# Kernel tuning notes

Measured on AMD Instinct MI355X. Metric: run time of the kernel, lower is better.

## Reference

```python
import jax, jax.numpy as jnp
import numpy as np

G = 4  # groupsize((1,1)) = 4 -> C4 rotations, exact rot90 path


def _lift_filter(w):
    # w: (O, I, k, k) -> (O*G, I, k, k); orbit of 90-degree filter rotations
    f = jnp.stack([jnp.rot90(w, r, axes=(-2, -1)) for r in range(G)], axis=1)
    O, _, I, k, _ = f.shape
    return f.reshape(O * G, I, k, k)


def _group_filter(w):
    # w: (O, I, G, k, k) -> (O*G, I*G, k, k)
    # rotatestack_n: spatial rot90 by r, then cyclic shift of the group axis by r
    fs = []
    for r in range(G):
        roty = jnp.rot90(w, r, axes=(-2, -1))
        roty = jnp.roll(roty, r, axis=-3)  # new[i] = roty[(G - r + i) % G]
        fs.append(roty)
    f = jnp.stack(fs, axis=1)  # (O, G, I, G, k, k)
    O, _, I, _, k, _ = f.shape
    return f.reshape(O * G, I * G, k, k)


def _conv(x, f, b, pad):
    y = jax.lax.conv_general_dilated(x, f, (1, 1), [(pad, pad), (pad, pad)],
                                     dimension_numbers=('NCHW', 'OIHW', 'NCHW'))
    # bias is stacked per group element: repeat each out-channel bias G times
    return y + jnp.repeat(b, G)[None, :, None, None]


def _pool(x):
    return jax.lax.reduce_window(x, -jnp.inf, jax.lax.max, (1, 1, 2, 2), (1, 1, 2, 2), 'VALID')


def setup_inputs():
    key = jax.random.key(0)
    ks = jax.random.split(key, 16)
    ch = [6, 12, 12, 24, 24, 16]   # [24,48,48,96,96,64] // G
    kern = [7, 5, 5, 5, 5, 5]
    d = {'x': jax.random.normal(ks[0], (64, 1, 96, 96), jnp.float32)}
    d['w0'] = jax.random.normal(ks[1], (ch[0], 1, kern[0], kern[0]), jnp.float32) / np.sqrt(ch[0] * 1.0)
    d['b0'] = jnp.zeros((ch[0],), jnp.float32)
    for i in range(1, 6):
        std = 1.0 / np.sqrt(float(ch[i] * ch[i - 1]))
        d['w%d' % i] = jax.random.normal(ks[1 + i], (ch[i], ch[i - 1], G, kern[i], kern[i]), jnp.float32) * std
        d['b%d' % i] = jnp.zeros((ch[i],), jnp.float32)
    d['fw1'] = jax.random.normal(ks[8], (64, 64), jnp.float32) * 0.05
    d['fb1'] = jnp.zeros((64,), jnp.float32)
    d['fw2'] = jax.random.normal(ks[9], (10, 64), jnp.float32) * 0.05
    d['fb2'] = jnp.zeros((10,), jnp.float32)
    return d


def reference(x, w0, b0, w1, b1, w2, b2, w3, b3, w4, b4, w5, b5, fw1, fb1, fw2, fb2):
    h = jax.nn.relu(_conv(x, _lift_filter(w0), b0, 1))                  # (B,24,92,92)
    h = jax.nn.relu(_conv(h, _group_filter(w1), b1, 2))
    h = _pool(h)                                                        # (B,48,46,46)
    h = jax.nn.relu(_conv(h, _group_filter(w2), b2, 2))
    h = jax.nn.relu(_conv(h, _group_filter(w3), b3, 2))
    h = _pool(h)                                                        # (B,96,23,23)
    h = jax.nn.relu(_conv(h, _group_filter(w4), b4, 2))
    h = jax.nn.relu(_conv(h, _group_filter(w5), b5, 1))                 # (B,64,21,21)
    h = h.mean(axis=(-2, -1))                                           # (B,64) flat (out_ch*G)
    h = jax.nn.relu(h @ fw1.T + fb1)
    return h @ fw2.T + fb2                                              # (B,10)
```

## Files before the change

kernel.cpp:

```cpp
#include <hip/hip_runtime.h>
#include <hip/hip_bf16.h>


typedef short s16x8 __attribute__((ext_vector_type(8)));
typedef __bf16 bf16x8 __attribute__((ext_vector_type(8)));
typedef float f32x4 __attribute__((ext_vector_type(4)));
typedef unsigned short u16;

__device__ __forceinline__ u16 f2bf(float f) {
    unsigned u = __float_as_uint(f);
    return (u16)((u + 0x7FFFu + ((u >> 16) & 1u)) >> 16);
}
__device__ __forceinline__ float bf2f(u16 h) {
    return __uint_as_float(((unsigned)h) << 16);
}

__device__ __forceinline__ void rot_src(int r, int K, int y, int x, int& sy, int& sx) {
    switch (r & 3) {
        case 0: sy = y;         sx = x;         break;
        case 1: sy = x;         sx = K - 1 - y; break;
        case 2: sy = K - 1 - y; sx = K - 1 - x; break;
        default: sy = K - 1 - x; sx = y;        break;
    }
}

__global__ void lift_w0T_kernel(const float* __restrict__ w, float* __restrict__ f) {
    const int K = 7, KK = 49, OC = 24;
    int idx = blockIdx.x * blockDim.x + threadIdx.x;
    if (idx >= KK * OC) return;
    int oc = idx % OC; int kk = idx / OC;
    int y = kk / K, x = kk % K;
    int r = oc & 3, o = oc >> 2;
    int sy, sx; rot_src(r, K, y, x, sy, sx);
    f[idx] = w[o * KK + sy * K + sx];
}

__global__ void wfrag_kernel(const float* __restrict__ w, u16* __restrict__ wf,
                             int O, int I, int KC, int NT, int total) {
    int idx = blockIdx.x * blockDim.x + threadIdx.x;
    if (idx >= total) return;
    int j = idx & 7;
    int lane = (idx >> 3) & 63;
    int rest = idx >> 9;
    int nc = rest % NT; rest /= NT;
    int kc = rest % KC; int kpos = rest / KC;
    int ky = kpos / 5, kx = kpos % 5;
    int kk = ((lane >> 4) << 3) + j;
    int ic = kc * 32 + kk;
    int oc = nc * 16 + (lane & 15);
    float val = 0.f;
    if (ic < I * 4) {
        int o = oc >> 2, r = oc & 3, i = ic >> 2, s = ic & 3;
        int g = (s - r + 4) & 3;
        int sy, sx; rot_src(r, 5, ky, kx, sy, sx);
        val = w[(((o * I + i) * 4 + g) * 25) + sy * 5 + sx];
    }
    u16 hb = f2bf(val);
    u16 lb = f2bf(val - bf2f(hb));
    wf[idx] = hb;
    wf[idx + total] = lb;
}

__global__ void pad_x_kernel(const float* __restrict__ x, float* __restrict__ xp) {
    int idx = blockIdx.x * blockDim.x + threadIdx.x;
    if (idx >= 64 * 96 * 96) return;
    int c = idx % 96; int t = idx / 96;
    int r = t % 96; int n = t / 96;
    xp[((size_t)n * 98 + r + 1) * 100 + c + 1] = x[idx];
}

__global__ void prep_pad_kernel(u16* __restrict__ buf, long LO, int NHW,
                                int Hp, int Wp, int ICO, int CR8) {
    int idx = blockIdx.x * blockDim.x + threadIdx.x;
    if (idx >= NHW) return;
    int c = idx % Wp; int t = idx / Wp;
    int r = t % Hp; int n = t / Hp;
    bool halo = (r < 2) || (r >= Hp - 2) || (c < 2) || (c >= Wp - 2);
    int c0 = halo ? 0 : CR8, c1 = ICO >> 3;
    if (c0 >= c1) return;
    size_t base = (((size_t)n * Hp + r) * Wp + c) * ICO;
    s16x8 z = {0, 0, 0, 0, 0, 0, 0, 0};
    for (int cc = c0; cc < c1; ++cc) {
        *(s16x8*)(buf + base + cc * 8) = z;
        *(s16x8*)(buf + LO + base + cc * 8) = z;
    }
}

__global__ __launch_bounds__(256) void conv0_kernel(
        const float* __restrict__ xp, const float* __restrict__ f0t,
        const float* __restrict__ b0, u16* __restrict__ p1, long p1LO) {
    int idx = blockIdx.x * blockDim.x + threadIdx.x;
    if (idx >= 64 * 92 * 23) return;
    int xq = idx % 23; int t = idx / 23;
    int oy = t % 92; int n = t / 92;
    float acc[24][4];
#pragma unroll
    for (int a = 0; a < 24; ++a)
#pragma unroll
        for (int b = 0; b < 4; ++b) acc[a][b] = 0.f;

    const float* ip = xp + ((size_t)n * 98 + oy) * 100 + xq * 4;
#pragma unroll
    for (int ky = 0; ky < 7; ++ky) {
        const float* row = ip + (size_t)ky * 100;
        float xv[12];
#pragma unroll
        for (int v = 0; v < 3; ++v)
            *reinterpret_cast<float4*>(&xv[4 * v]) =
                *reinterpret_cast<const float4*>(row + 4 * v);
#pragma unroll
        for (int kx = 0; kx < 7; ++kx) {
            const float* wp = f0t + (ky * 7 + kx) * 24;
#pragma unroll
            for (int qd = 0; qd < 6; ++qd) {
                float4 wv = *reinterpret_cast<const float4*>(wp + qd * 4);
#pragma unroll
                for (int jx = 0; jx < 4; ++jx) {
                    acc[qd * 4 + 0][jx] = fmaf(wv.x, xv[kx + jx], acc[qd * 4 + 0][jx]);
                    acc[qd * 4 + 1][jx] = fmaf(wv.y, xv[kx + jx], acc[qd * 4 + 1][jx]);
                    acc[qd * 4 + 2][jx] = fmaf(wv.z, xv[kx + jx], acc[qd * 4 + 2][jx]);
                    acc[qd * 4 + 3][jx] = fmaf(wv.w, xv[kx + jx], acc[qd * 4 + 3][jx]);
                }
            }
        }
    }
    float bv[6];
#pragma unroll
    for (int qd = 0; qd < 6; ++qd) bv[qd] = b0[qd];

    size_t ob = (((size_t)n * 96 + oy + 2) * 96 + xq * 4 + 2) * 32;
#pragma unroll
    for (int jx = 0; jx < 4; ++jx) {
        s16x8 hv[4], lv[4];
#pragma unroll
        for (int cc = 0; cc < 3; ++cc)
#pragma unroll
            for (int e = 0; e < 8; ++e) {
                int ch = cc * 8 + e;
                float v = fmaxf(acc[ch][jx] + bv[ch >> 2], 0.f);
                u16 hb = f2bf(v);
                u16 lb = f2bf(v - bf2f(hb));
                hv[cc][e] = (short)hb; lv[cc][e] = (short)lb;
            }
        hv[3] = s16x8{0,0,0,0,0,0,0,0}; lv[3] = s16x8{0,0,0,0,0,0,0,0};
#pragma unroll
        for (int cc = 0; cc < 4; ++cc) {
            *(s16x8*)(p1 + ob + jx * 32 + cc * 8) = hv[cc];
            *(s16x8*)(p1 + p1LO + ob + jx * 32 + cc * 8) = lv[cc];
        }
    }
}

template <int IC32, int NT, int NTW, int MT, int CR, int SW, bool POOL, int XOFF>
__global__ __launch_bounds__(SW*(NT/NTW)*64, 2) void conv_mfma_kernel(
        const u16* __restrict__ act, long actLO,
        const u16* __restrict__ wf, int wfLO,
        const float* __restrict__ bias,
        u16* __restrict__ outP, long outLO,
        float* __restrict__ outF,
        int Hp, int Wp, int OH, int OW, int PH, int POW,
        int NRG, int NXS, int HpO, int WpO, int IC32O) {
    constexpr int OG = NT / NTW;
    constexpr int NW = SW * OG;
    constexpr int KC = IC32 / 32;
    constexpr int WT = MT * 16 + 4 + XOFF;
    constexpr int R  = CR * SW + 4;
    constexpr int CHUNKS = R * WT * 8;
    __shared__ u16 lds[CHUNKS * 8];

    int q8 = gridDim.x >> 3;
    int wid = (blockIdx.x & 7) * q8 + (blockIdx.x >> 3);
    int xs = wid % NXS; int t = wid / NXS;
    int rgrp = t % NRG; int n = t / NRG;

    int BR = rgrp * (CR * SW);
    int rbase = BR + XOFF;
    int xbase = xs * (MT * 16);

    int tid = threadIdx.x;
    int wv = tid >> 6;
    int lane = tid & 63;
    int l15 = lane & 15, lg = lane >> 4;
    int og = wv % OG, rg = wv / OG;

    f32x4 accP[CR][MT][NTW], accQ[CR][MT][NTW];
#pragma unroll
    for (int cr = 0; cr < CR; ++cr)
#pragma unroll
        for (int m = 0; m < MT; ++m)
#pragma unroll
            for (int nc = 0; nc < NTW; ++nc) {
                accP[cr][m][nc] = f32x4{0.f, 0.f, 0.f, 0.f};
                accQ[cr][m][nc] = f32x4{0.f, 0.f, 0.f, 0.f};
            }

    const u16* wfl = wf + (size_t)lane * 8;
    const u16* actn = act + ((size_t)n * Hp) * Wp * IC32;

    for (int kcp = 0; kcp < KC; ++kcp) {
        if (kcp) __syncthreads();
        for (int u = tid; u < CHUNKS; u += NW * 64) {
            int c = u & 7; int rest = u >> 3;
            int xl = rest % WT; int row = rest / WT;
            int cg = c ^ (xl & 7);
            int sp = cg >> 2, cc4 = cg & 3;
            int gx = xbase + xl, gr = rbase + row;
            s16x8 v = {0, 0, 0, 0, 0, 0, 0, 0};
            if (gx < Wp && gr < Hp)
                v = *(const s16x8*)(actn + (size_t)sp * actLO +
                      ((size_t)gr * Wp + gx) * IC32 + (kcp * 4 + cc4) * 8);
            *(s16x8*)&lds[(size_t)u * 8] = v;
        }
        __syncthreads();

        for (int ky = 0; ky < 5; ++ky) {
            for (int kx = 0; kx < 5; ++kx) {
                int kpos = ky * 5 + kx;
                bf16x8 bh[NTW], bl[NTW];
#pragma unroll
                for (int nc = 0; nc < NTW; ++nc) {
                    const u16* bp = wfl +
                        ((size_t)(kpos * KC + kcp) * NT + og * NTW + nc) * 512;
                    bh[nc] = *(const bf16x8*)bp;
                    bl[nc] = *(const bf16x8*)(bp + wfLO);
                }
#pragma unroll
                for (int m = 0; m < MT; ++m) {
                    int xl = m * 16 + XOFF + l15 + kx;
                    int sw = xl & 7;
                    bf16x8 ah[CR], al[CR];
#pragma unroll
                    for (int cr = 0; cr < CR; ++cr) {
                        int row = rg * CR + cr + ky;
                        int base = (row * WT + xl) * 8;
                        ah[cr] = *(const bf16x8*)&lds[(size_t)(base + (lg ^ sw)) * 8];
                        al[cr] = *(const bf16x8*)&lds[(size_t)(base + ((4 + lg) ^ sw)) * 8];
                    }
#pragma unroll
                    for (int nc = 0; nc < NTW; ++nc)
#pragma unroll
                        for (int cr = 0; cr < CR; ++cr) {
                            accP[cr][m][nc] = __builtin_amdgcn_mfma_f32_16x16x32_bf16(
                                ah[cr], bh[nc], accP[cr][m][nc], 0, 0, 0);
                            accQ[cr][m][nc] = __builtin_amdgcn_mfma_f32_16x16x32_bf16(
                                ah[cr], bl[nc], accQ[cr][m][nc], 0, 0, 0);
                            accQ[cr][m][nc] = __builtin_amdgcn_mfma_f32_16x16x32_bf16(
                                al[cr], bh[nc], accQ[cr][m][nc], 0, 0, 0);
                        }
                }
            }
        }
    }

#pragma unroll
    for (int nc = 0; nc < NTW; ++nc) {
        int oc = (og * NTW + nc) * 16 + l15;
        float bv = bias[oc >> 2];
#pragma unroll
        for (int m = 0; m < MT; ++m) {
            int gx0 = xbase + m * 16;
            if constexpr (POOL) {
                int p = rgrp * SW + rg;
                if (p < PH) {
                    float c0[4], c1[4];
#pragma unroll
                    for (int j = 0; j < 4; ++j) {
                        c0[j] = accP[0][m][nc][j] + accQ[0][m][nc][j];
                        c1[j] = accP[1][m][nc][j] + accQ[1][m][nc][j];
                    }
#pragma unroll
                    for (int a2 = 0; a2 < 2; ++a2) {
                        int px = (gx0 + lg * 4 + 2 * a2) >> 1;
                        if (px < POW) {
                            float mx = fmaxf(fmaxf(c0[2 * a2], c0[2 * a2 + 1]),
                                             fmaxf(c1[2 * a2], c1[2 * a2 + 1]));
                            float v = fmaxf(mx + bv, 0.f);
                            u16 hb = f2bf(v);
                            u16 lb = f2bf(v - bf2f(hb));
                            size_t o = (((size_t)n * HpO + p + 2) * WpO + px + 2) * IC32O + oc;
                            outP[o] = hb; outP[o + outLO] = lb;
                        }
                    }
                }
            } else {
#pragma unroll
                for (int cr = 0; cr < CR; ++cr) {
                    int oy = BR + rg * CR + cr;
                    if (oy < OH) {
#pragma unroll
                        for (int j = 0; j < 4; ++j) {
                            int gx = gx0 + lg * 4 + j;
                            if (gx < OW) {
                                float v = fmaxf(accP[cr][m][nc][j] + accQ[cr][m][nc][j] + bv, 0.f);
                                if (outF) {
                                    outF[(((size_t)n * OH + oy) * OW + gx) * (NT * 16) + oc] = v;
                                } else {
                                    u16 hb = f2bf(v);
                                    u16 lb = f2bf(v - bf2f(hb));
                                    size_t o = (((size_t)n * HpO + oy + 2) * WpO + gx + 2) * IC32O + oc;
                                    outP[o] = hb; outP[o + outLO] = lb;
                                }
                            }
                        }
                    }
                }
            }
        }
    }
}

__global__ void mean_nhwc_kernel(const float* __restrict__ in, float* __restrict__ out) {
    __shared__ float sm[256];
    int n = blockIdx.x;
    int c = threadIdx.x & 63, q = threadIdx.x >> 6;
    float s = 0.f;
    for (int p = q; p < 441; p += 4) s += in[((size_t)n * 441 + p) * 64 + c];
    sm[threadIdx.x] = s;
    __syncthreads();
    if (q == 0) out[n * 64 + c] = (sm[c] + sm[c + 64] + sm[c + 128] + sm[c + 192]) * (1.0f / 441.0f);
}

__global__ void fc_kernel(const float* __restrict__ mean, const float* __restrict__ fw1,
                          const float* __restrict__ fb1, const float* __restrict__ fw2,
                          const float* __restrict__ fb2, float* __restrict__ out) {
    __shared__ float m[4096];
    __shared__ float h1[4096];
    int tid = threadIdx.x;
    for (int i = tid; i < 4096; i += 256) m[i] = mean[i];
    __syncthreads();
    for (int i = tid; i < 4096; i += 256) {
        int n = i >> 6, j = i & 63;
        float s = fb1[j];
        for (int k = 0; k < 64; ++k) s = fmaf(m[n * 64 + k], fw1[j * 64 + k], s);
        h1[i] = fmaxf(s, 0.f);
    }
    __syncthreads();
    for (int i = tid; i < 640; i += 256) {
        int n = i / 10, j2 = i % 10;
        float s = fb2[j2];
        for (int j = 0; j < 64; ++j) s = fmaf(h1[n * 64 + j], fw2[j2 * 64 + j], s);
        out[i] = s;
    }
}

extern "C" void kernel_launch(void* const* d_in, const int* in_sizes, int n_in,
                              void* d_out, int out_size, void* d_ws, size_t ws_size,
                              hipStream_t stream) {
    const float* x   = (const float*)d_in[0];
    const float* w0  = (const float*)d_in[1];
    const float* b0  = (const float*)d_in[2];
    const float* w1  = (const float*)d_in[3];
    const float* b1  = (const float*)d_in[4];
    const float* w2  = (const float*)d_in[5];
    const float* b2  = (const float*)d_in[6];
    const float* w3  = (const float*)d_in[7];
    const float* b3  = (const float*)d_in[8];
    const float* w4  = (const float*)d_in[9];
    const float* b4  = (const float*)d_in[10];
    const float* w5  = (const float*)d_in[11];
    const float* b5  = (const float*)d_in[12];
    const float* fw1 = (const float*)d_in[13];
    const float* fb1 = (const float*)d_in[14];
    const float* fw2 = (const float*)d_in[15];
    const float* fb2 = (const float*)d_in[16];

    char* ws = (char*)d_ws;
    if (ws_size < 128827392ull) return;

    float* F0   = (float*)(ws + 0);
    u16*   WF1  = (u16*)(ws + 8192);
    u16*   WF2  = (u16*)(ws + 161792);
    u16*   WF3  = (u16*)(ws + 468992);
    u16*   WF4  = (u16*)(ws + 1083392);
    u16*   WF5  = (u16*)(ws + 2004992);
    float* MEANB= (float*)(ws + 2619392);
    float* XP   = (float*)(ws + 2635776);
    float* C5   = (float*)(ws + 5144576);
    u16*   A    = (u16*)(ws + 12369920);
    u16*   B    = (u16*)(ws + 87867392);
    const long P1LO = 18874368;
    const long P2LO = 10240000;
    const long P4LO = 4478976;

    hipLaunchKernelGGL(lift_w0T_kernel, dim3(5), dim3(256), 0, stream, w0, F0);
    hipLaunchKernelGGL(wfrag_kernel, dim3(150), dim3(256), 0, stream, w1, WF1, 12, 6, 1, 3, 38400);
    hipLaunchKernelGGL(wfrag_kernel, dim3(300), dim3(256), 0, stream, w2, WF2, 12, 12, 2, 3, 76800);
    hipLaunchKernelGGL(wfrag_kernel, dim3(600), dim3(256), 0, stream, w3, WF3, 24, 12, 2, 6, 153600);
    hipLaunchKernelGGL(wfrag_kernel, dim3(900), dim3(256), 0, stream, w4, WF4, 24, 24, 3, 6, 230400);
    hipLaunchKernelGGL(wfrag_kernel, dim3(600), dim3(256), 0, stream, w5, WF5, 16, 24, 3, 4, 153600);

    hipMemsetAsync(XP, 0, 2508800, stream);
    hipLaunchKernelGGL(pad_x_kernel, dim3(2304), dim3(256), 0, stream, x, XP);

    hipLaunchKernelGGL(prep_pad_kernel, dim3((64*96*96 + 255)/256), dim3(256), 0, stream,
                       A, P1LO, 64*96*96, 96, 96, 32, 4);
    hipLaunchKernelGGL(conv0_kernel, dim3((64*92*23 + 255)/256), dim3(256), 0, stream,
                       XP, F0, b0, A, P1LO);

    hipLaunchKernelGGL(prep_pad_kernel, dim3((64*50*50 + 255)/256), dim3(256), 0, stream,
                       B, P2LO, 64*50*50, 50, 50, 64, 6);
    hipLaunchKernelGGL((conv_mfma_kernel<32, 3, 3, 3, 2, 4, true, 0>), dim3(1536), dim3(256), 0, stream,
                       A, P1LO, WF1, 38400, b1, B, P2LO, (float*)nullptr,
                       96, 96, 92, 92, 46, 46, 12, 2, 50, 50, 64);

    hipLaunchKernelGGL(prep_pad_kernel, dim3((64*50*50 + 255)/256), dim3(256), 0, stream,
                       A, P2LO, 64*50*50, 50, 50, 64, 6);
    hipLaunchKernelGGL((conv_mfma_kernel<64, 3, 3, 3, 1, 4, false, 0>), dim3(768), dim3(256), 0, stream,
                       B, P2LO, WF2, 76800, b2, A, P2LO, (float*)nullptr,
                       50, 50, 46, 46, 0, 0, 12, 1, 50, 50, 64);

    hipLaunchKernelGGL(prep_pad_kernel, dim3((64*27*27 + 255)/256), dim3(256), 0, stream,
                       B, P4LO, 64*27*27, 27, 27, 96, 12);
    hipLaunchKernelGGL((conv_mfma_kernel<64, 6, 3, 3, 2, 2, true, 0>), dim3(768), dim3(256), 0, stream,
                       A, P2LO, WF3, 153600, b3, B, P4LO, (float*)nullptr,
                       50, 50, 46, 46, 23, 23, 12, 1, 27, 27, 96);

    hipLaunchKernelGGL(prep_pad_kernel, dim3((64*27*27 + 255)/256), dim3(256), 0, stream,
                       A, P4LO, 64*27*27, 27, 27, 96, 12);
    hipLaunchKernelGGL((conv_mfma_kernel<96, 6, 3, 2, 2, 2, false, 0>), dim3(384), dim3(256), 0, stream,
                       B, P4LO, WF4, 230400, b4, A, P4LO, (float*)nullptr,
                       27, 27, 23, 23, 0, 0, 6, 1, 27, 27, 96);

    hipLaunchKernelGGL((conv_mfma_kernel<96, 4, 2, 2, 2, 2, false, 1>), dim3(384), dim3(256), 0, stream,
                       A, P4LO, WF5, 153600, b5, (u16*)A, 0, C5,
                       27, 27, 21, 21, 0, 0, 6, 1, 27, 27, 96);

    hipLaunchKernelGGL(mean_nhwc_kernel, dim3(64), dim3(256), 0, stream, C5, MEANB);
    hipLaunchKernelGGL(fc_kernel, dim3(1), dim3(256), 0, stream,
                       MEANB, fw1, fb1, fw2, fb2, (float*)d_out);
}
```

Before: 677.4 us.

## Stage conv epilogue through LDS for coalesced vector stores and shrink padded buffers

Conv epilogues now write their bf16 hi/lo results into shared memory first, then write them out to the padded NHWC buffer with 16-byte coalesced stores, instead of scattered 2-byte stores. The first activation buffer is stored with 24 channels instead of zero-padded 32, and the conv kernel zero-fills the missing channels when loading. The prep kernels now zero only the halo. The main conv loops are fully unrolled and occupancy hints are raised for some layers. The LDS staging adds an extra barrier and shared-memory traffic, and the unrolling may raise register pressure.

New measurement: 1.478 ms. 2.18x slower.

```diff
diff --git a/kernel.cpp b/kernel.cpp
--- a/kernel.cpp
+++ b/kernel.cpp
@@ -6,6 +6,7 @@
 typedef __bf16 bf16x8 __attribute__((ext_vector_type(8)));
 typedef float f32x4 __attribute__((ext_vector_type(4)));
 typedef unsigned short u16;
+typedef unsigned int u32;
 
 __device__ __forceinline__ u16 f2bf(float f) {
     unsigned u = __float_as_uint(f);
@@ -69,18 +70,17 @@
     xp[((size_t)n * 98 + r + 1) * 100 + c + 1] = x[idx];
 }
 
-__global__ void prep_pad_kernel(u16* __restrict__ buf, long LO, int NHW,
-                                int Hp, int Wp, int ICO, int CR8) {
+__global__ void prep_halo_kernel(u16* __restrict__ buf, long LO, int NHW,
+                                 int Hp, int Wp, int ICO) {
     int idx = blockIdx.x * blockDim.x + threadIdx.x;
     if (idx >= NHW) return;
     int c = idx % Wp; int t = idx / Wp;
     int r = t % Hp; int n = t / Hp;
     bool halo = (r < 2) || (r >= Hp - 2) || (c < 2) || (c >= Wp - 2);
-    int c0 = halo ? 0 : CR8, c1 = ICO >> 3;
-    if (c0 >= c1) return;
+    if (!halo) return;
     size_t base = (((size_t)n * Hp + r) * Wp + c) * ICO;
     s16x8 z = {0, 0, 0, 0, 0, 0, 0, 0};
-    for (int cc = c0; cc < c1; ++cc) {
+    for (int cc = 0; cc < (ICO >> 3); ++cc) {
         *(s16x8*)(buf + base + cc * 8) = z;
         *(s16x8*)(buf + LO + base + cc * 8) = z;
     }
@@ -128,10 +128,10 @@
 #pragma unroll
     for (int qd = 0; qd < 6; ++qd) bv[qd] = b0[qd];
 
-    size_t ob = (((size_t)n * 96 + oy + 2) * 96 + xq * 4 + 2) * 32;
+    size_t ob = (((size_t)n * 96 + oy + 2) * 96 + xq * 4 + 2) * 24;
 #pragma unroll
     for (int jx = 0; jx < 4; ++jx) {
-        s16x8 hv[4], lv[4];
+        s16x8 hv[3], lv[3];
 #pragma unroll
         for (int cc = 0; cc < 3; ++cc)
 #pragma unroll
@@ -142,36 +142,43 @@
                 u16 lb = f2bf(v - bf2f(hb));
                 hv[cc][e] = (short)hb; lv[cc][e] = (short)lb;
             }
-        hv[3] = s16x8{0,0,0,0,0,0,0,0}; lv[3] = s16x8{0,0,0,0,0,0,0,0};
-#pragma unroll
-        for (int cc = 0; cc < 4; ++cc) {
-            *(s16x8*)(p1 + ob + jx * 32 + cc * 8) = hv[cc];
-            *(s16x8*)(p1 + p1LO + ob + jx * 32 + cc * 8) = lv[cc];
-        }
-    }
-}
-
-template <int IC32, int NT, int NTW, int MT, int CR, int SW, bool POOL, int XOFF>
-__global__ __launch_bounds__(SW*(NT/NTW)*64, 2) void conv_mfma_kernel(
+#pragma unroll
+        for (int cc = 0; cc < 3; ++cc) {
+            *(s16x8*)(p1 + ob + jx * 24 + cc * 8) = hv[cc];
+            *(s16x8*)(p1 + p1LO + ob + jx * 24 + cc * 8) = lv[cc];
+        }
+    }
+}
+
+template <int IC32, int ICIN, int NT, int NTW, int MT, int CR, int SW, bool POOL,
+          int XOFF, int OCO, bool TRANS, int MINW>
+__global__ __launch_bounds__(SW*(NT/NTW)*64, MINW) void conv_mfma_kernel(
         const u16* __restrict__ act, long actLO,
         const u16* __restrict__ wf, int wfLO,
         const float* __restrict__ bias,
         u16* __restrict__ outP, long outLO,
         float* __restrict__ outF,
         int Hp, int Wp, int OH, int OW, int PH, int POW,
-        int NRG, int NXS, int HpO, int WpO, int IC32O) {
+        int NRG, int NXS, int HpO, int WpO) {
     constexpr int OG = NT / NTW;
     constexpr int NW = SW * OG;
     constexpr int KC = IC32 / 32;
     constexpr int WT = MT * 16 + 4 + XOFF;
     constexpr int R  = CR * SW + 4;
     constexpr int CHUNKS = R * WT * 8;
-    __shared__ u16 lds[CHUNKS * 8];
+    constexpr int TROWS = POOL ? SW : CR * SW;
+    constexpr int TX = POOL ? MT * 8 : MT * 16;
+    constexpr int SX = OCO + 4;
+    constexpr int STAGE_B = CHUNKS * 16;
+    constexpr int TRAN_B = TRANS ? TROWS * TX * SX * 4 : 0;
+    constexpr int LDSB = STAGE_B > TRAN_B ? STAGE_B : TRAN_B;
+    __shared__ __align__(16) char ldsraw[LDSB];
+    u16* lds = (u16*)ldsraw;
 
     int q8 = gridDim.x >> 3;
     int wid = (blockIdx.x & 7) * q8 + (blockIdx.x >> 3);
-    int xs = wid % NXS; int t = wid / NXS;
-    int rgrp = t % NRG; int n = t / NRG;
+    int xs = wid % NXS; int t0 = wid / NXS;
+    int rgrp = t0 % NRG; int n = t0 / NRG;
 
     int BR = rgrp * (CR * SW);
     int rbase = BR + XOFF;
@@ -195,7 +202,7 @@
             }
 
     const u16* wfl = wf + (size_t)lane * 8;
-    const u16* actn = act + ((size_t)n * Hp) * Wp * IC32;
+    const u16* actn = act + ((size_t)n * Hp) * Wp * ICIN;
 
     for (int kcp = 0; kcp < KC; ++kcp) {
         if (kcp) __syncthreads();
@@ -205,15 +212,18 @@
             int cg = c ^ (xl & 7);
             int sp = cg >> 2, cc4 = cg & 3;
             int gx = xbase + xl, gr = rbase + row;
+            int ch0 = (kcp * 4 + cc4) * 8;
             s16x8 v = {0, 0, 0, 0, 0, 0, 0, 0};
-            if (gx < Wp && gr < Hp)
+            if (gx < Wp && gr < Hp && ch0 < ICIN)
                 v = *(const s16x8*)(actn + (size_t)sp * actLO +
-                      ((size_t)gr * Wp + gx) * IC32 + (kcp * 4 + cc4) * 8);
+                      ((size_t)gr * Wp + gx) * ICIN + ch0);
             *(s16x8*)&lds[(size_t)u * 8] = v;
         }
         __syncthreads();
 
+#pragma unroll
         for (int ky = 0; ky < 5; ++ky) {
+#pragma unroll
             for (int kx = 0; kx < 5; ++kx) {
                 int kpos = ky * 5 + kx;
                 bf16x8 bh[NTW], bl[NTW];
@@ -252,16 +262,16 @@
         }
     }
 
-#pragma unroll
-    for (int nc = 0; nc < NTW; ++nc) {
-        int oc = (og * NTW + nc) * 16 + l15;
-        float bv = bias[oc >> 2];
-#pragma unroll
-        for (int m = 0; m < MT; ++m) {
-            int gx0 = xbase + m * 16;
-            if constexpr (POOL) {
-                int p = rgrp * SW + rg;
-                if (p < PH) {
+    if constexpr (TRANS) {
+        __syncthreads();
+        u32* ldsw = (u32*)ldsraw;
+#pragma unroll
+        for (int nc = 0; nc < NTW; ++nc) {
+            int oc = (og * NTW + nc) * 16 + l15;
+            float bv = bias[oc >> 2];
+#pragma unroll
+            for (int m = 0; m < MT; ++m) {
+                if constexpr (POOL) {
                     float c0[4], c1[4];
 #pragma unroll
                     for (int j = 0; j < 4; ++j) {
@@ -270,19 +280,70 @@
                     }
 #pragma unroll
                     for (int a2 = 0; a2 < 2; ++a2) {
-                        int px = (gx0 + lg * 4 + 2 * a2) >> 1;
-                        if (px < POW) {
-                            float mx = fmaxf(fmaxf(c0[2 * a2], c0[2 * a2 + 1]),
-                                             fmaxf(c1[2 * a2], c1[2 * a2 + 1]));
-                            float v = fmaxf(mx + bv, 0.f);
+                        float mx = fmaxf(fmaxf(c0[2 * a2], c0[2 * a2 + 1]),
+                                         fmaxf(c1[2 * a2], c1[2 * a2 + 1]));
+                        float v = fmaxf(mx + bv, 0.f);
+                        u16 hb = f2bf(v);
+                        u16 lb = f2bf(v - bf2f(hb));
+                        int px = m * 8 + lg * 2 + a2;
+                        ldsw[(rg * TX + px) * SX + oc] = ((u32)hb << 16) | lb;
+                    }
+                } else {
+#pragma unroll
+                    for (int cr = 0; cr < CR; ++cr)
+#pragma unroll
+                        for (int j = 0; j < 4; ++j) {
+                            float v = fmaxf(accP[cr][m][nc][j] + accQ[cr][m][nc][j] + bv, 0.f);
                             u16 hb = f2bf(v);
                             u16 lb = f2bf(v - bf2f(hb));
-                            size_t o = (((size_t)n * HpO + p + 2) * WpO + px + 2) * IC32O + oc;
-                            outP[o] = hb; outP[o + outLO] = lb;
+                            int xloc = m * 16 + lg * 4 + j;
+                            ldsw[((rg * CR + cr) * TX + xloc) * SX + oc] =
+                                ((u32)hb << 16) | lb;
                         }
-                    }
-                }
-            } else {
+                }
+            }
+        }
+        __syncthreads();
+        constexpr int CPX = OCO / 8;
+        constexpr int TOT = TROWS * TX * 2 * CPX;
+        int OHL = POOL ? PH : OH;
+        int OWL = POOL ? POW : OW;
+        int obr = POOL ? rgrp * SW : BR;
+        int obx = POOL ? (xbase >> 1) : xbase;
+        for (int u = tid; u < TOT; u += NW * 64) {
+            int c = u % CPX; int rest = u / CPX;
+            int pl = rest & 1; rest >>= 1;
+            int x = rest % TX; int row = rest / TX;
+            int gr = obr + row, gx = obx + x;
+            if (gr >= OHL || gx >= OWL) continue;
+            s16x8 v = {0, 0, 0, 0, 0, 0, 0, 0};
+            if (c * 8 < NT * 16) {
+                const u32* p = &ldsw[(row * TX + x) * SX + c * 8];
+                uint4 w0 = *(const uint4*)p;
+                uint4 w1 = *(const uint4*)(p + 4);
+                if (pl == 0) {
+                    v[0] = (short)(w0.x >> 16); v[1] = (short)(w0.y >> 16);
+                    v[2] = (short)(w0.z >> 16); v[3] = (short)(w0.w >> 16);
+                    v[4] = (short)(w1.x >> 16); v[5] = (short)(w1.y >> 16);
+                    v[6] = (short)(w1.z >> 16); v[7] = (short)(w1.w >> 16);
+                } else {
+                    v[0] = (short)(w0.x & 0xffff); v[1] = (short)(w0.y & 0xffff);
+                    v[2] = (short)(w0.z & 0xffff); v[3] = (short)(w0.w & 0xffff);
+                    v[4] = (short)(w1.x & 0xffff); v[5] = (short)(w1.y & 0xffff);
+                    v[6] = (short)(w1.z & 0xffff); v[7] = (short)(w1.w & 0xffff);
+                }
+            }
+            *(s16x8*)(outP + (size_t)pl * outLO +
+                      (((size_t)n * HpO + gr + 2) * WpO + gx + 2) * OCO + c * 8) = v;
+        }
+    } else {
+#pragma unroll
+        for (int nc = 0; nc < NTW; ++nc) {
+            int oc = (og * NTW + nc) * 16 + l15;
+            float bv = bias[oc >> 2];
+#pragma unroll
+            for (int m = 0; m < MT; ++m) {
+                int gx0 = xbase + m * 16;
 #pragma unroll
                 for (int cr = 0; cr < CR; ++cr) {
                     int oy = BR + rg * CR + cr;
@@ -292,14 +353,7 @@
                             int gx = gx0 + lg * 4 + j;
                             if (gx < OW) {
                                 float v = fmaxf(accP[cr][m][nc][j] + accQ[cr][m][nc][j] + bv, 0.f);
-                                if (outF) {
-                                    outF[(((size_t)n * OH + oy) * OW + gx) * (NT * 16) + oc] = v;
-                                } else {
-                                    u16 hb = f2bf(v);
-                                    u16 lb = f2bf(v - bf2f(hb));
-                                    size_t o = (((size_t)n * HpO + oy + 2) * WpO + gx + 2) * IC32O + oc;
-                                    outP[o] = hb; outP[o + outLO] = lb;
-                                }
+                                outF[(((size_t)n * OH + oy) * OW + gx) * (NT * 16) + oc] = v;
                             }
                         }
                     }
@@ -378,7 +432,7 @@
     float* C5   = (float*)(ws + 5144576);
     u16*   A    = (u16*)(ws + 12369920);
     u16*   B    = (u16*)(ws + 87867392);
-    const long P1LO = 18874368;
+    const long P1LO = 14155776;
     const long P2LO = 10240000;
     const long P4LO = 4478976;
 
@@ -392,38 +446,43 @@
     hipMemsetAsync(XP, 0, 2508800, stream);
     hipLaunchKernelGGL(pad_x_kernel, dim3(2304), dim3(256), 0, stream, x, XP);
 
-    hipLaunchKernelGGL(prep_pad_kernel, dim3((64*96*96 + 255)/256), dim3(256), 0, stream,
-                       A, P1LO, 64*96*96, 96, 96, 32, 4);
+    hipLaunchKernelGGL(prep_halo_kernel, dim3(2304), dim3(256), 0, stream,
+                       A, P1LO, 64*96*96, 96, 96, 24);
     hipLaunchKernelGGL(conv0_kernel, dim3((64*92*23 + 255)/256), dim3(256), 0, stream,
                        XP, F0, b0, A, P1LO);
 
-    hipLaunchKernelGGL(prep_pad_kernel, dim3((64*50*50 + 255)/256), dim3(256), 0, stream,
-                       B, P2LO, 64*50*50, 50, 50, 64, 6);
-    hipLaunchKernelGGL((conv_mfma_kernel<32, 3, 3, 3, 2, 4, true, 0>), dim3(1536), dim3(256), 0, stream,
+    hipLaunchKernelGGL(prep_halo_kernel, dim3(625), dim3(256), 0, stream,
+                       B, P2LO, 64*50*50, 50, 50, 64);
+    hipLaunchKernelGGL((conv_mfma_kernel<32, 24, 3, 3, 3, 2, 4, true, 0, 64, true, 2>),
+                       dim3(1536), dim3(256), 0, stream,
                        A, P1LO, WF1, 38400, b1, B, P2LO, (float*)nullptr,
-                       96, 96, 92, 92, 46, 46, 12, 2, 50, 50, 64);
-
-    hipLaunchKernelGGL(prep_pad_kernel, dim3((64*50*50 + 255)/256), dim3(256), 0, stream,
-                       A, P2LO, 64*50*50, 50, 50, 64, 6);
-    hipLaunchKernelGGL((conv_mfma_kernel<64, 3, 3, 3, 1, 4, false, 0>), dim3(768), dim3(256), 0, stream,
+                       96, 96, 92, 92, 46, 46, 12, 2, 50, 50);
+
+    hipLaunchKernelGGL(prep_halo_kernel, dim3(625), dim3(256), 0, stream,
+                       A, P2LO, 64*50*50, 50, 50, 64);
+    hipLaunchKernelGGL((conv_mfma_kernel<64, 64, 3, 3, 3, 1, 4, false, 0, 64, true, 3>),
+                       dim3(768), dim3(256), 0, stream,
                        B, P2LO, WF2, 76800, b2, A, P2LO, (float*)nullptr,
-                       50, 50, 46, 46, 0, 0, 12, 1, 50, 50, 64);
-
-    hipLaunchKernelGGL(prep_pad_kernel, dim3((64*27*27 + 255)/256), dim3(256), 0, stream,
-                       B, P4LO, 64*27*27, 27, 27, 96, 12);
-    hipLaunchKernelGGL((conv_mfma_kernel<64, 6, 3, 3, 2, 2, true, 0>), dim3(768), dim3(256), 0, stream,
+                       50, 50, 46, 46, 0, 0, 12, 1, 50, 50);
+
+    hipLaunchKernelGGL(prep_halo_kernel, dim3(183), dim3(256), 0, stream,
+                       B, P4LO, 64*27*27, 27, 27, 96);
+    hipLaunchKernelGGL((conv_mfma_kernel<64, 64, 6, 3, 3, 2, 2, true, 0, 96, true, 2>),
+                       dim3(768), dim3(256), 0, stream,
                        A, P2LO, WF3, 153600, b3, B, P4LO, (float*)nullptr,
-                       50, 50, 46, 46, 23, 23, 12, 1, 27, 27, 96);
-
-    hipLaunchKernelGGL(prep_pad_kernel, dim3((64*27*27 + 255)/256), dim3(256), 0, stream,
-                       A, P4LO, 64*27*27, 27, 27, 96, 12);
-    hipLaunchKernelGGL((conv_mfma_kernel<96, 6, 3, 2, 2, 2, false, 0>), dim3(384), dim3(256), 0, stream,
+                       50, 50, 46, 46, 23, 23, 12, 1, 27, 27);
+
+    hipLaunchKernelGGL(prep_halo_kernel, dim3(183), dim3(256), 0, stream,
+                       A, P4LO, 64*27*27, 27, 27, 96);
+    hipLaunchKernelGGL((conv_mfma_kernel<96, 96, 6, 3, 2, 2, 2, false, 0, 96, true, 3>),
+                       dim3(384), dim3(256), 0, stream,
                        B, P4LO, WF4, 230400, b4, A, P4LO, (float*)nullptr,
-                       27, 27, 23, 23, 0, 0, 6, 1, 27, 27, 96);
-
-    hipLaunchKernelGGL((conv_mfma_kernel<96, 4, 2, 2, 2, 2, false, 1>), dim3(384), dim3(256), 0, stream,
+                       27, 27, 23, 23, 0, 0, 6, 1, 27, 27);
+
+    hipLaunchKernelGGL((conv_mfma_kernel<96, 96, 4, 2, 2, 2, 2, false, 1, 96, false, 3>),
+                       dim3(384), dim3(256), 0, stream,
                        A, P4LO, WF5, 153600, b5, (u16*)A, 0, C5,
-                       27, 27, 21, 21, 0, 0, 6, 1, 27, 27, 96);
+                       27, 27, 21, 21, 0, 0, 6, 1, 27, 27);
 
     hipLaunchKernelGGL(mean_nhwc_kernel, dim3(64), dim3(256), 0, stream, C5, MEANB);
     hipLaunchKernelGGL(fc_kernel, dim3(1), dim3(256), 0, stream,
```
